# Optimization experiments

Measured on AMD Instinct MI355X. Metric: run time of the kernel, lower is better.

The kernel has to match this reference:

```python
import jax, jax.numpy as jnp
import numpy as np

MODEL_DIM = 1024
NUM_HEADS = 16
HEAD_DIM = MODEL_DIM // NUM_HEADS
B, SQ, SK = 1, 4096, 4096


def setup_inputs() -> dict:
    key = jax.random.key(0)
    ks = jax.random.split(key, 10)
    s = 0.02  # realistic init scale for weights
    inp = {
        "x_query": jax.random.normal(ks[0], (B, SQ, MODEL_DIM), jnp.float32),
        "x_context": jax.random.normal(ks[1], (B, SK, MODEL_DIM), jnp.float32),
        # causal mask [B,1,Sq,Sk]; 0 -> masked
        "mask": jnp.tril(jnp.ones((SQ, SK), jnp.int32))[None, None, :, :],
        "wq": jax.random.normal(ks[2], (MODEL_DIM, MODEL_DIM), jnp.float32) * s,
        "bq": jnp.zeros((MODEL_DIM,), jnp.float32),
        "wk": jax.random.normal(ks[3], (MODEL_DIM, MODEL_DIM), jnp.float32) * s,
        "bk": jnp.zeros((MODEL_DIM,), jnp.float32),
        "wv": jax.random.normal(ks[4], (MODEL_DIM, MODEL_DIM), jnp.float32) * s,
        "bv": jnp.zeros((MODEL_DIM,), jnp.float32),
        "wo": jax.random.normal(ks[5], (MODEL_DIM, MODEL_DIM), jnp.float32) * s,
        "bo": jnp.zeros((MODEL_DIM,), jnp.float32),
    }
    return inp


def reference(x_query, x_context, mask, wq, bq, wk, bk, wv, bv, wo, bo):
    b = x_query.shape[0]
    # torch nn.Linear: y = x @ W.T + b
    q = x_query @ wq.T + bq
    k = x_context @ wk.T + bk
    v = x_context @ wv.T + bv
    # [B, S, D] -> [B, H, S, Hd]
    def split_heads(t):
        return t.reshape(b, -1, NUM_HEADS, HEAD_DIM).transpose(0, 2, 1, 3)
    q, k, v = split_heads(q), split_heads(k), split_heads(v)
    scale = 1.0 / jnp.sqrt(jnp.asarray(HEAD_DIM, q.dtype))
    scores = jnp.einsum('bhqd,bhkd->bhqk', q, k) * scale  # [B,H,Sq,Sk]
    scores = jnp.where(mask == 0, jnp.asarray(-1e9, scores.dtype), scores)
    attn = jax.nn.softmax(scores, axis=-1)
    # dropout: eval mode (identity)
    ctx = jnp.einsum('bhqk,bhkd->bhqd', attn, v)
    ctx = ctx.transpose(0, 2, 1, 3).reshape(b, -1, MODEL_DIM)
    return ctx @ wo.T + bo
```

## Files before the change

### kernel.cpp

```cpp
#include <hip/hip_runtime.h>

typedef __bf16 bf16x8 __attribute__((ext_vector_type(8)));
typedef float f32x4 __attribute__((ext_vector_type(4)));
typedef float f32x16 __attribute__((ext_vector_type(16)));
typedef unsigned int u32x2v __attribute__((ext_vector_type(2)));

#define GLD16(gp, lp) __builtin_amdgcn_global_load_lds( \
    (const __attribute__((address_space(1))) void*)(gp), \
    (__attribute__((address_space(3))) void*)(lp), 16, 0, 0)

__device__ __forceinline__ unsigned short f2bf(float f) {
  unsigned int u = __float_as_uint(f);
  u += 0x7FFFu + ((u >> 16) & 1u);
  return (unsigned short)(u >> 16);
}

__device__ __forceinline__ unsigned int cvtpk(float lo, float hi) {
  unsigned int r;
  asm("v_cvt_pk_bf16_f32 %0, %1, %2" : "=v"(r) : "v"(lo), "v"(hi));
  return r;
}

__device__ __forceinline__ float exp2f_(float x) {
#if __has_builtin(__builtin_amdgcn_exp2f)
  return __builtin_amdgcn_exp2f(x);
#else
  float r; asm("v_exp_f32 %0, %1" : "=v"(r) : "v"(x)); return r;
#endif
}

__device__ __forceinline__ u32x2v pswap(unsigned int a, unsigned int b) {
#if __has_builtin(__builtin_amdgcn_permlane32_swap)
  u32x2v r;
  auto q = __builtin_amdgcn_permlane32_swap(a, b, false, false);
  r[0] = q[0]; r[1] = q[1];
  return r;
#else
  unsigned int pa = (unsigned int)__shfl_xor((int)a, 32);
  unsigned int pb = (unsigned int)__shfl_xor((int)b, 32);
  int hi = (threadIdx.x >> 5) & 1;
  u32x2v r;
  r[0] = hi ? pb : a;
  r[1] = hi ? b : pa;
  return r;
#endif
}

__global__ __launch_bounds__(256) void cast6(
    const float* __restrict__ xq, const float* __restrict__ xc,
    const float* __restrict__ wq, const float* __restrict__ wk,
    const float* __restrict__ wv, const float* __restrict__ wo,
    unsigned short* __restrict__ d) {
  int i = (blockIdx.x * 256 + threadIdx.x) * 4;
  const float* s; int off;
  if      (i < (4 << 20))  { s = xq; off = 0; }
  else if (i < (8 << 20))  { s = xc; off = 4 << 20; }
  else if (i < (9 << 20))  { s = wq; off = 8 << 20; }
  else if (i < (10 << 20)) { s = wk; off = 9 << 20; }
  else if (i < (11 << 20)) { s = wv; off = 10 << 20; }
  else                     { s = wo; off = 11 << 20; }
  float4 v = *(const float4*)(s + (i - off));
  ushort4 o;
  o.x = f2bf(v.x); o.y = f2bf(v.y); o.z = f2bf(v.z); o.w = f2bf(v.w);
  *(ushort4*)(d + i) = o;
}

template<int OUTF32>
__device__ __forceinline__ void gemm_body(
    const unsigned short* __restrict__ A, const unsigned short* __restrict__ B,
    const float* __restrict__ bias, void* __restrict__ C,
    int N, int K, int bm, int bn, float scale,
    unsigned short* As, unsigned short* Bs) {
  const int t = threadIdx.x;
  const int lane = t & 63, wid = t >> 6;
  const int wm = wid >> 1, wn = wid & 1;
  const int l15 = lane & 15, l4 = lane >> 4, l7 = lane & 7;

  f32x4 acc[2][4];
#pragma unroll
  for (int i = 0; i < 2; ++i)
#pragma unroll
    for (int j = 0; j < 4; ++j) acc[i][j] = (f32x4){0.f, 0.f, 0.f, 0.f};

  const char* Ab = (const char*)A;
  const char* Bb = (const char*)B;
  const int ldb = K * 2;

  for (int kt = 0; kt < K; kt += 64) {
#pragma unroll
    for (int c = 0; c < 2; ++c) {
      int id = c * 512 + t;
      int row = id >> 3;
      int ch = (id & 7) ^ (row & 7);
      const char* ga = Ab + (size_t)(bm * 128 + row) * ldb + kt * 2 + ch * 16;
      GLD16(ga, (char*)As + id * 16);
      const char* gb = Bb + (size_t)(bn * 128 + row) * ldb + kt * 2 + ch * 16;
      GLD16(gb, (char*)Bs + id * 16);
    }
    __syncthreads();
#pragma unroll
    for (int kk = 0; kk < 2; ++kk) {
      bf16x8 af[2], bfr[4];
#pragma unroll
      for (int mi = 0; mi < 2; ++mi) {
        int row = wm * 32 + mi * 16 + l15;
        int ch = (l4 + 4 * kk) ^ l7;
        af[mi] = *(const bf16x8*)((const char*)As + row * 128 + ch * 16);
      }
#pragma unroll
      for (int ni = 0; ni < 4; ++ni) {
        int row = wn * 64 + ni * 16 + l15;
        int ch = (l4 + 4 * kk) ^ l7;
        bfr[ni] = *(const bf16x8*)((const char*)Bs + row * 128 + ch * 16);
      }
#pragma unroll
      for (int mi = 0; mi < 2; ++mi)
#pragma unroll
        for (int ni = 0; ni < 4; ++ni)
          acc[mi][ni] = __builtin_amdgcn_mfma_f32_16x16x32_bf16(
              af[mi], bfr[ni], acc[mi][ni], 0, 0, 0);
    }
    __syncthreads();
  }

#pragma unroll
  for (int ni = 0; ni < 4; ++ni) {
    int col = bn * 128 + wn * 64 + ni * 16 + l15;
    float bv = bias[col];
#pragma unroll
    for (int mi = 0; mi < 2; ++mi) {
#pragma unroll
      for (int r = 0; r < 4; ++r) {
        int row = bm * 128 + wm * 32 + mi * 16 + l4 * 4 + r;
        float v = (acc[mi][ni][r] + bv) * scale;
        if (OUTF32) ((float*)C)[(size_t)row * N + col] = v;
        else ((unsigned short*)C)[(size_t)row * N + col] = f2bf(v);
      }
    }
  }
}

__global__ __launch_bounds__(512) void gemm_qkv(
    const unsigned short* __restrict__ xq, const unsigned short* __restrict__ xc,
    const unsigned short* __restrict__ wq, const unsigned short* __restrict__ wk,
    const unsigned short* __restrict__ wv,
    const float* __restrict__ bq, const float* __restrict__ bk,
    const float* __restrict__ bv,
    unsigned short* __restrict__ Qo, unsigned short* __restrict__ Ko,
    unsigned short* __restrict__ Vo) {
  __shared__ __align__(16) unsigned short As[128 * 64];
  __shared__ __align__(16) unsigned short Bs[128 * 64];
  const unsigned short* A; const unsigned short* B; const float* bias;
  unsigned short* C; float scale;
  if (blockIdx.z == 0)      { A = xq; B = wq; bias = bq; C = Qo; scale = 0.18033688011112042f; }
  else if (blockIdx.z == 1) { A = xc; B = wk; bias = bk; C = Ko; scale = 1.0f; }
  else                      { A = xc; B = wv; bias = bv; C = Vo; scale = 1.0f; }
  int flat = blockIdx.x + 8 * blockIdx.y;
  int tid = (flat & 7) * 32 + (flat >> 3);
  int bm = tid >> 3, bn = tid & 7;
  gemm_body<0>(A, B, bias, (void*)C, 1024, 1024, bm, bn, scale, As, Bs);
}

__global__ __launch_bounds__(512) void gemm_out(
    const unsigned short* __restrict__ A, const unsigned short* __restrict__ B,
    const float* __restrict__ bias, float* __restrict__ C) {
  __shared__ __align__(16) unsigned short As[64 * 64];
  __shared__ __align__(16) unsigned short Bs[128 * 64];
  int flat = blockIdx.x + 8 * blockIdx.y;
  int tid = (flat & 7) * 64 + (flat >> 3);
  const int bm = tid >> 3, bn = tid & 7;
  const int t = threadIdx.x;
  const int lane = t & 63, wid = t >> 6;
  const int wm = wid >> 2, wn = wid & 3;
  const int l15 = lane & 15, l4 = lane >> 4, l7 = lane & 7;

  f32x4 acc[2][2];
#pragma unroll
  for (int i = 0; i < 2; ++i)
#pragma unroll
    for (int j = 0; j < 2; ++j) acc[i][j] = (f32x4){0.f, 0.f, 0.f, 0.f};

  const char* Ab = (const char*)A;
  const char* Bb = (const char*)B;
  const int ldb = 2048;

  for (int kt = 0; kt < 1024; kt += 64) {
    {
      int id = t;
      int row = id >> 3;
      int ch = (id & 7) ^ (row & 7);
      const char* ga = Ab + (size_t)(bm * 64 + row) * ldb + kt * 2 + ch * 16;
      GLD16(ga, (char*)As + id * 16);
    }
#pragma unroll
    for (int c = 0; c < 2; ++c) {
      int id = c * 512 + t;
      int row = id >> 3;
      int ch = (id & 7) ^ (row & 7);
      const char* gb = Bb + (size_t)(bn * 128 + row) * ldb + kt * 2 + ch * 16;
      GLD16(gb, (char*)Bs + id * 16);
    }
    __syncthreads();
#pragma unroll
    for (int kk = 0; kk < 2; ++kk) {
      bf16x8 af[2], bfr[2];
#pragma unroll
      for (int mi = 0; mi < 2; ++mi) {
        int row = wm * 32 + mi * 16 + l15;
        int ch = (l4 + 4 * kk) ^ l7;
        af[mi] = *(const bf16x8*)((const char*)As + row * 128 + ch * 16);
      }
#pragma unroll
      for (int ni = 0; ni < 2; ++ni) {
        int row = wn * 32 + ni * 16 + l15;
        int ch = (l4 + 4 * kk) ^ l7;
        bfr[ni] = *(const bf16x8*)((const char*)Bs + row * 128 + ch * 16);
      }
#pragma unroll
      for (int mi = 0; mi < 2; ++mi)
#pragma unroll
        for (int ni = 0; ni < 2; ++ni)
          acc[mi][ni] = __builtin_amdgcn_mfma_f32_16x16x32_bf16(
              af[mi], bfr[ni], acc[mi][ni], 0, 0, 0);
    }
    __syncthreads();
  }

#pragma unroll
  for (int ni = 0; ni < 2; ++ni) {
    int col = bn * 128 + wn * 32 + ni * 16 + l15;
    float bv = bias[col];
#pragma unroll
    for (int mi = 0; mi < 2; ++mi) {
#pragma unroll
      for (int r = 0; r < 4; ++r) {
        int row = bm * 64 + wm * 32 + mi * 16 + l4 * 4 + r;
        C[(size_t)row * 1024 + col] = acc[mi][ni][r] + bv;
      }
    }
  }
}

__global__ __launch_bounds__(256)
void flash_attn(
    const unsigned short* __restrict__ Q, const unsigned short* __restrict__ K,
    const unsigned short* __restrict__ V, unsigned short* __restrict__ O,
    unsigned short* __restrict__ partO, float* __restrict__ lBase) {
  __shared__ __align__(16) char smem[32768];

  const int b = blockIdx.x;
  const int h = b & 15;
  const int ep = b >> 4;
  int qb, role, P;
  if (ep < 30)      { qb = 31 - ep / 3; role = ep % 3; P = 3; }
  else if (ep < 52) { int k = ep - 30; qb = 21 - (k >> 1); role = k & 1; P = 2; }
  else              { qb = 10 - (ep - 52); role = 0; P = 1; }

  const int T = 2 * qb + 2;
  const int t0 = (role * T) / P;
  const int n  = ((role + 1) * T) / P - t0;

  const int t = threadIdx.x;
  const int lane = t & 63, w = t >> 6;
  const int l31 = lane & 31, hi = lane >> 5;
  const int q0w = qb * 128 + w * 32;
  const int qwmax = q0w + 31;

  bf16x8 qf[4];
#pragma unroll
  for (int ks = 0; ks < 4; ++ks)
    qf[ks] = *(const bf16x8*)(Q + (size_t)(q0w + l31) * 1024 + h * 64 + ks * 16 + hi * 8);

  f32x16 po0, po1;
#pragma unroll
  for (int r = 0; r < 16; ++r) { po0[r] = 0.f; po1[r] = 0.f; }
  float lacc[8];
#pragma unroll
  for (int i = 0; i < 8; ++i) lacc[i] = 0.f;

  const int vd4 = (t & 15) * 4;
  const int vkvr = (t >> 4) * 4;
  uint2 va[4];

  auto stageK = [&](int tile, int buf) {
#pragma unroll
    for (int i = 0; i < 2; ++i) {
      int id = i * 256 + t;
      int row = id >> 3;
      int ch = (id & 7) ^ (row & 7);
      GLD16((const char*)K + (size_t)(tile * 64 + row) * 2048 + h * 128 + ch * 16,
            smem + buf * 8192 + id * 16);
    }
  };
  auto loadV = [&](int tile) {
#pragma unroll
    for (int i = 0; i < 4; ++i)
      va[i] = *(const uint2*)(V + (size_t)(tile * 64 + vkvr + i) * 1024 + h * 64 + vd4);
  };
  auto writeV = [&](int buf) {
    char* Vt = smem + 16384 + buf * 8192;
#pragma unroll
    for (int j = 0; j < 4; ++j) {
      unsigned sel = (j & 1) ? 0x07060302u : 0x05040100u;
      unsigned s01 = (j < 2) ? __builtin_amdgcn_perm(va[1].x, va[0].x, sel)
                             : __builtin_amdgcn_perm(va[1].y, va[0].y, sel);
      unsigned s23 = (j < 2) ? __builtin_amdgcn_perm(va[3].x, va[2].x, sel)
                             : __builtin_amdgcn_perm(va[3].y, va[2].y, sel);
      int row = vd4 + j;
      int sw = (vkvr * 2) ^ (((row >> 2) & 7) << 4);
      *(uint2*)(Vt + row * 128 + sw) = make_uint2(s01, s23);
    }
  };

  stageK(t0, 0);
  loadV(t0);
  writeV(0);
  __syncthreads();

  for (int it = 0; it < n; ++it) {
    const int c = it & 1;
    const bool pf = (it + 1) < n;
    if (pf) { stageK(t0 + it + 1, c ^ 1); loadV(t0 + it + 1); }

    const int kv0 = (t0 + it) * 64;
    if (kv0 <= qwmax) {
      const char* Ks = smem + c * 8192;
      const char* Vt = smem + 16384 + c * 8192;
      f32x16 s0, s1;
#pragma unroll
      for (int r = 0; r < 16; ++r) { s0[r] = 0.f; s1[r] = 0.f; }
      __builtin_amdgcn_s_setprio(1);
#pragma unroll
      for (int ks = 0; ks < 4; ++ks) {
        int c0 = ((ks * 2 + hi) ^ (l31 & 7)) << 4;
        bf16x8 k0 = *(const bf16x8*)(Ks + l31 * 128 + c0);
        bf16x8 k1 = *(const bf16x8*)(Ks + (32 + l31) * 128 + c0);
        s0 = __builtin_amdgcn_mfma_f32_32x32x16_bf16(k0, qf[ks], s0, 0, 0, 0);
        s1 = __builtin_amdgcn_mfma_f32_32x32x16_bf16(k1, qf[ks], s1, 0, 0, 0);
      }
      __builtin_amdgcn_s_setprio(0);
      if (kv0 + 63 > q0w) {
        int q = q0w + l31;
#pragma unroll
        for (int r = 0; r < 16; ++r) {
          int kvi = kv0 + (r & 3) + 8 * (r >> 2) + 4 * hi;
          if (kvi > q) s0[r] = -1e30f;
          if (kvi + 32 > q) s1[r] = -1e30f;
        }
      }
#pragma unroll
      for (int r = 0; r < 16; ++r) s0[r] = exp2f_(s0[r]);
#pragma unroll
      for (int r = 0; r < 16; ++r) s1[r] = exp2f_(s1[r]);
#pragma unroll
      for (int i = 0; i < 8; ++i)
        lacc[i] += (s0[2 * i] + s0[2 * i + 1]) + (s1[2 * i] + s1[2 * i + 1]);

#pragma unroll
      for (int kp = 0; kp < 4; ++kp) {
        const f32x16& sv = (kp < 2) ? s0 : s1;
        const int bb = (kp & 1) * 8;
        unsigned c0v = cvtpk(sv[bb + 0], sv[bb + 1]);
        unsigned c1v = cvtpk(sv[bb + 2], sv[bb + 3]);
        unsigned c2v = cvtpk(sv[bb + 4], sv[bb + 5]);
        unsigned c3v = cvtpk(sv[bb + 6], sv[bb + 7]);
        u32x2v w02 = pswap(c0v, c2v);
        u32x2v w13 = pswap(c1v, c3v);
        union { unsigned u[4]; bf16x8 v; } pfr;
        pfr.u[0] = w02[0]; pfr.u[1] = w13[0]; pfr.u[2] = w02[1]; pfr.u[3] = w13[1];
        int cb = kp * 2 + hi;
        __builtin_amdgcn_s_setprio(1);
        {
          int row = l31;
          bf16x8 vf = *(const bf16x8*)(Vt + row * 128 + ((cb ^ ((row >> 2) & 7)) << 4));
          po0 = __builtin_amdgcn_mfma_f32_32x32x16_bf16(vf, pfr.v, po0, 0, 0, 0);
        }
        {
          int row = 32 + l31;
          bf16x8 vf = *(const bf16x8*)(Vt + row * 128 + ((cb ^ ((row >> 2) & 7)) << 4));
          po1 = __builtin_amdgcn_mfma_f32_32x32x16_bf16(vf, pfr.v, po1, 0, 0, 0);
        }
        __builtin_amdgcn_s_setprio(0);
      }
    }
    if (pf) writeV(c ^ 1);
    __syncthreads();
  }

  float l4v[4];
#pragma unroll
  for (int i = 0; i < 4; ++i) l4v[i] = lacc[i] + lacc[4 + i];
  float ps = (l4v[0] + l4v[1]) + (l4v[2] + l4v[3]);
  u32x2v sw2 = pswap(__float_as_uint(ps), __float_as_uint(ps));
  const float l_i = __uint_as_float(sw2[0]) + __uint_as_float(sw2[1]);
  const float rinv = 1.0f / l_i;

  if (P > 1) {
    const int slot = h * 52 + ep;
    unsigned u[16];
#pragma unroll
    for (int i = 0; i < 8; ++i) u[i] = cvtpk(po0[2 * i] * rinv, po0[2 * i + 1] * rinv);
#pragma unroll
    for (int i = 0; i < 8; ++i) u[8 + i] = cvtpk(po1[2 * i] * rinv, po1[2 * i + 1] * rinv);
    char* bO = (char*)partO + (size_t)slot * 16384 + t * 64;
    *(uint4*)(bO +  0) = make_uint4(u[0], u[1], u[2], u[3]);
    *(uint4*)(bO + 16) = make_uint4(u[4], u[5], u[6], u[7]);
    *(uint4*)(bO + 32) = make_uint4(u[8], u[9], u[10], u[11]);
    *(uint4*)(bO + 48) = make_uint4(u[12], u[13], u[14], u[15]);
    if (!hi) {
      lBase[(size_t)slot * 128 + w * 32 + l31] = l_i;
    }
    return;
  }

  {
    int qlocal = w * 32 + l31;
#pragma unroll
    for (int g = 0; g < 4; ++g) {
#pragma unroll
      for (int db = 0; db < 2; ++db) {
        const f32x16& p = db ? po1 : po0;
        unsigned w0 = cvtpk(p[g * 4 + 0] * rinv, p[g * 4 + 1] * rinv);
        unsigned w1 = cvtpk(p[g * 4 + 2] * rinv, p[g * 4 + 3] * rinv);
        int d0 = db * 32 + 8 * g + 4 * hi;
        int byte = qlocal * 128 + ((d0 * 2) ^ ((qlocal & 7) << 4));
        *(uint2*)(smem + byte) = make_uint2(w0, w1);
      }
    }
  }
  __syncthreads();
#pragma unroll
  for (int it = 0; it < 4; ++it) {
    int r = it * 32 + (t >> 3);
    int c = t & 7;
    uint4 val = *(const uint4*)(smem + r * 128 + ((c ^ (r & 7)) << 4));
    *(uint4*)((char*)O + (size_t)(qb * 128 + r) * 2048 + h * 128 + c * 16) = val;
  }
}

__global__ __launch_bounds__(256) void flash_merge(
    const unsigned short* __restrict__ partO, const float* __restrict__ lBase,
    unsigned short* __restrict__ O) {
  const int p = blockIdx.x;
  const int h = p & 15;
  const int j = p >> 4;
  int qb, P, e0;
  if (j < 10) { qb = 31 - j; P = 3; e0 = j * 3; }
  else        { qb = 21 - (j - 10); P = 2; e0 = 30 + (j - 10) * 2; }
  const int t = threadIdx.x;
  const int s = t >> 6, hi = (t >> 5) & 1, l31 = t & 31;

  float acc[32];
#pragma unroll
  for (int i = 0; i < 32; ++i) acc[i] = 0.f;
  float den = 0.f;
#pragma unroll
  for (int r = 0; r < 3; ++r) {
    if (r < P) {
      float wgt = lBase[(size_t)(h * 52 + e0 + r) * 128 + s * 32 + l31];
      den += wgt;
      const uint4* bO = (const uint4*)((const char*)partO +
                         (size_t)(h * 52 + e0 + r) * 16384 + t * 64);
      uint4 a = bO[0], b2 = bO[1], c2 = bO[2], d2 = bO[3];
      unsigned uu[16] = {a.x, a.y, a.z, a.w, b2.x, b2.y, b2.z, b2.w,
                         c2.x, c2.y, c2.z, c2.w, d2.x, d2.y, d2.z, d2.w};
#pragma unroll
      for (int i = 0; i < 16; ++i) {
        acc[2 * i]     += wgt * __uint_as_float(uu[i] << 16);
        acc[2 * i + 1] += wgt * __uint_as_float(uu[i] & 0xFFFF0000u);
      }
    }
  }
  float rinv = 1.0f / den;
  const int q = qb * 128 + s * 32 + l31;
  unsigned short* orow = O + (size_t)q * 1024 + h * 64;
#pragma unroll
  for (int r = 0; r < 16; ++r) {
    int d = (r & 3) + 8 * (r >> 2) + 4 * hi;
    orow[d]      = f2bf(acc[r] * rinv);
    orow[d + 32] = f2bf(acc[16 + r] * rinv);
  }
}

extern "C" void kernel_launch(void* const* d_in, const int* in_sizes, int n_in,
                              void* d_out, int out_size, void* d_ws, size_t ws_size,
                              hipStream_t stream) {
  const float* xq = (const float*)d_in[0];
  const float* xc = (const float*)d_in[1];
  const float* wq = (const float*)d_in[3];
  const float* bq = (const float*)d_in[4];
  const float* wk = (const float*)d_in[5];
  const float* bk = (const float*)d_in[6];
  const float* wv = (const float*)d_in[7];
  const float* bv = (const float*)d_in[8];
  const float* wo = (const float*)d_in[9];
  const float* bo = (const float*)d_in[10];

  unsigned short* wsb = (unsigned short*)d_ws;
  unsigned short* xqb = wsb;
  unsigned short* xcb = wsb + (4 << 20);
  unsigned short* wqb = wsb + (8 << 20);
  unsigned short* wkb = wsb + (9 << 20);
  unsigned short* wvb = wsb + (10 << 20);
  unsigned short* wob = wsb + (11 << 20);
  unsigned short* Qb  = wsb + (12 << 20);
  unsigned short* Kb  = wsb + (16 << 20);
  unsigned short* Vb  = wsb + (20 << 20);
  unsigned short* Cb  = wsb + (24 << 20);

  unsigned short* partO = (unsigned short*)d_ws;
  float* lBase = (float*)((char*)d_ws + (14u << 20));

  cast6<<<12288, 256, 0, stream>>>(xq, xc, wq, wk, wv, wo, wsb);

  dim3 gq(1024 / 128, 4096 / 128, 3);
  gemm_qkv<<<gq, 512, 0, stream>>>(xqb, xcb, wqb, wkb, wvb, bq, bk, bv, Qb, Kb, Vb);

  flash_attn<<<1008, 256, 0, stream>>>(Qb, Kb, Vb, Cb, partO, lBase);

  flash_merge<<<336, 256, 0, stream>>>(partO, lBase, Cb);

  dim3 go(1024 / 128, 4096 / 64);
  gemm_out<<<go, 512, 0, stream>>>(Cb, wob, bo, (float*)d_out);
}
```

Measured before the change: 140.1 us.

## Fuse activation fp32-to-bf16 cast into QKV GEMM A-tile loads

Stops pre-casting x_query and x_context to bf16 in a separate pass. The QKV GEMM now loads fp32 A tiles straight into LDS with a new swizzle and converts them to bf16 with v_cvt_pk_bf16_f32 when building fragments. Only the weights are still cast ahead of time. This removes a 32 MB read plus 16 MB write pass. In exchange, A-tile global and LDS traffic inside the GEMM doubles, LDS use grows to 48 KB per block, and the conversion adds ALU work in the inner loop that K and V blocks repeat on the same rows.

Result: slower. 148.7 us (+6.1%).

```diff
diff --git a/kernel.cpp b/kernel.cpp
--- a/kernel.cpp
+++ b/kernel.cpp
@@ -46,111 +46,33 @@
 #endif
 }
 
-__global__ __launch_bounds__(256) void cast6(
-    const float* __restrict__ xq, const float* __restrict__ xc,
+__global__ __launch_bounds__(256) void cast_w(
     const float* __restrict__ wq, const float* __restrict__ wk,
     const float* __restrict__ wv, const float* __restrict__ wo,
     unsigned short* __restrict__ d) {
   int i = (blockIdx.x * 256 + threadIdx.x) * 4;
   const float* s; int off;
-  if      (i < (4 << 20))  { s = xq; off = 0; }
-  else if (i < (8 << 20))  { s = xc; off = 4 << 20; }
-  else if (i < (9 << 20))  { s = wq; off = 8 << 20; }
-  else if (i < (10 << 20)) { s = wk; off = 9 << 20; }
-  else if (i < (11 << 20)) { s = wv; off = 10 << 20; }
-  else                     { s = wo; off = 11 << 20; }
+  if      (i < (1 << 20)) { s = wq; off = 0; }
+  else if (i < (2 << 20)) { s = wk; off = 1 << 20; }
+  else if (i < (3 << 20)) { s = wv; off = 2 << 20; }
+  else                    { s = wo; off = 3 << 20; }
   float4 v = *(const float4*)(s + (i - off));
   ushort4 o;
   o.x = f2bf(v.x); o.y = f2bf(v.y); o.z = f2bf(v.z); o.w = f2bf(v.w);
   *(ushort4*)(d + i) = o;
 }
 
-template<int OUTF32>
-__device__ __forceinline__ void gemm_body(
-    const unsigned short* __restrict__ A, const unsigned short* __restrict__ B,
-    const float* __restrict__ bias, void* __restrict__ C,
-    int N, int K, int bm, int bn, float scale,
-    unsigned short* As, unsigned short* Bs) {
-  const int t = threadIdx.x;
-  const int lane = t & 63, wid = t >> 6;
-  const int wm = wid >> 1, wn = wid & 1;
-  const int l15 = lane & 15, l4 = lane >> 4, l7 = lane & 7;
-
-  f32x4 acc[2][4];
-#pragma unroll
-  for (int i = 0; i < 2; ++i)
-#pragma unroll
-    for (int j = 0; j < 4; ++j) acc[i][j] = (f32x4){0.f, 0.f, 0.f, 0.f};
-
-  const char* Ab = (const char*)A;
-  const char* Bb = (const char*)B;
-  const int ldb = K * 2;
-
-  for (int kt = 0; kt < K; kt += 64) {
-#pragma unroll
-    for (int c = 0; c < 2; ++c) {
-      int id = c * 512 + t;
-      int row = id >> 3;
-      int ch = (id & 7) ^ (row & 7);
-      const char* ga = Ab + (size_t)(bm * 128 + row) * ldb + kt * 2 + ch * 16;
-      GLD16(ga, (char*)As + id * 16);
-      const char* gb = Bb + (size_t)(bn * 128 + row) * ldb + kt * 2 + ch * 16;
-      GLD16(gb, (char*)Bs + id * 16);
-    }
-    __syncthreads();
-#pragma unroll
-    for (int kk = 0; kk < 2; ++kk) {
-      bf16x8 af[2], bfr[4];
-#pragma unroll
-      for (int mi = 0; mi < 2; ++mi) {
-        int row = wm * 32 + mi * 16 + l15;
-        int ch = (l4 + 4 * kk) ^ l7;
-        af[mi] = *(const bf16x8*)((const char*)As + row * 128 + ch * 16);
-      }
-#pragma unroll
-      for (int ni = 0; ni < 4; ++ni) {
-        int row = wn * 64 + ni * 16 + l15;
-        int ch = (l4 + 4 * kk) ^ l7;
-        bfr[ni] = *(const bf16x8*)((const char*)Bs + row * 128 + ch * 16);
-      }
-#pragma unroll
-      for (int mi = 0; mi < 2; ++mi)
-#pragma unroll
-        for (int ni = 0; ni < 4; ++ni)
-          acc[mi][ni] = __builtin_amdgcn_mfma_f32_16x16x32_bf16(
-              af[mi], bfr[ni], acc[mi][ni], 0, 0, 0);
-    }
-    __syncthreads();
-  }
-
-#pragma unroll
-  for (int ni = 0; ni < 4; ++ni) {
-    int col = bn * 128 + wn * 64 + ni * 16 + l15;
-    float bv = bias[col];
-#pragma unroll
-    for (int mi = 0; mi < 2; ++mi) {
-#pragma unroll
-      for (int r = 0; r < 4; ++r) {
-        int row = bm * 128 + wm * 32 + mi * 16 + l4 * 4 + r;
-        float v = (acc[mi][ni][r] + bv) * scale;
-        if (OUTF32) ((float*)C)[(size_t)row * N + col] = v;
-        else ((unsigned short*)C)[(size_t)row * N + col] = f2bf(v);
-      }
-    }
-  }
-}
-
 __global__ __launch_bounds__(512) void gemm_qkv(
-    const unsigned short* __restrict__ xq, const unsigned short* __restrict__ xc,
+    const float* __restrict__ xq, const float* __restrict__ xc,
     const unsigned short* __restrict__ wq, const unsigned short* __restrict__ wk,
     const unsigned short* __restrict__ wv,
     const float* __restrict__ bq, const float* __restrict__ bk,
     const float* __restrict__ bv,
     unsigned short* __restrict__ Qo, unsigned short* __restrict__ Ko,
     unsigned short* __restrict__ Vo) {
-  __shared__ __align__(16) unsigned short As[128 * 64];
+  __shared__ __align__(16) float As[128 * 64];
   __shared__ __align__(16) unsigned short Bs[128 * 64];
-  const unsigned short* A; const unsigned short* B; const float* bias;
+  const float* A; const unsigned short* B; const float* bias;
   unsigned short* C; float scale;
   if (blockIdx.z == 0)      { A = xq; B = wq; bias = bq; C = Qo; scale = 0.18033688011112042f; }
   else if (blockIdx.z == 1) { A = xc; B = wk; bias = bk; C = Ko; scale = 1.0f; }
@@ -158,7 +80,86 @@
   int flat = blockIdx.x + 8 * blockIdx.y;
   int tid = (flat & 7) * 32 + (flat >> 3);
   int bm = tid >> 3, bn = tid & 7;
-  gemm_body<0>(A, B, bias, (void*)C, 1024, 1024, bm, bn, scale, As, Bs);
+
+  const int t = threadIdx.x;
+  const int lane = t & 63, wid = t >> 6;
+  const int wm = wid >> 1, wn = wid & 1;
+  const int l15 = lane & 15, l4 = lane >> 4, l7 = lane & 7;
+
+  f32x4 acc[2][4];
+#pragma unroll
+  for (int i = 0; i < 2; ++i)
+#pragma unroll
+    for (int j = 0; j < 4; ++j) acc[i][j] = (f32x4){0.f, 0.f, 0.f, 0.f};
+
+  const char* Bb = (const char*)B;
+
+  for (int kt = 0; kt < 1024; kt += 64) {
+#pragma unroll
+    for (int c = 0; c < 2; ++c) {
+      int id = c * 512 + t;
+      int row = id >> 3;
+      int ch = (id & 7) ^ (row & 7);
+      GLD16(Bb + (size_t)(bn * 128 + row) * 2048 + kt * 2 + ch * 16,
+            (char*)Bs + id * 16);
+    }
+#pragma unroll
+    for (int c = 0; c < 4; ++c) {
+      int id = c * 512 + t;
+      int row = id >> 4;
+      int cc = id & 15;
+      int sc = (((cc >> 1) ^ (row & 7)) << 1) | (cc & 1);
+      GLD16(A + (size_t)(bm * 128 + row) * 1024 + kt + sc * 4,
+            (char*)As + id * 16);
+    }
+    __syncthreads();
+#pragma unroll
+    for (int kk = 0; kk < 2; ++kk) {
+      bf16x8 af[2], bfr[4];
+#pragma unroll
+      for (int mi = 0; mi < 2; ++mi) {
+        int row = wm * 32 + mi * 16 + l15;
+        int p = (l4 + 4 * kk) ^ (row & 7);
+        const char* base = (const char*)As + row * 256 + p * 32;
+        f32x4 v0 = *(const f32x4*)(base);
+        f32x4 v1 = *(const f32x4*)(base + 16);
+        union { uint4 u; bf16x8 v; } cv;
+        cv.u.x = cvtpk(v0[0], v0[1]);
+        cv.u.y = cvtpk(v0[2], v0[3]);
+        cv.u.z = cvtpk(v1[0], v1[1]);
+        cv.u.w = cvtpk(v1[2], v1[3]);
+        af[mi] = cv.v;
+      }
+#pragma unroll
+      for (int ni = 0; ni < 4; ++ni) {
+        int row = wn * 64 + ni * 16 + l15;
+        int ch = (l4 + 4 * kk) ^ l7;
+        bfr[ni] = *(const bf16x8*)((const char*)Bs + row * 128 + ch * 16);
+      }
+#pragma unroll
+      for (int mi = 0; mi < 2; ++mi)
+#pragma unroll
+        for (int ni = 0; ni < 4; ++ni)
+          acc[mi][ni] = __builtin_amdgcn_mfma_f32_16x16x32_bf16(
+              af[mi], bfr[ni], acc[mi][ni], 0, 0, 0);
+    }
+    __syncthreads();
+  }
+
+#pragma unroll
+  for (int ni = 0; ni < 4; ++ni) {
+    int col = bn * 128 + wn * 64 + ni * 16 + l15;
+    float bv = bias[col];
+#pragma unroll
+    for (int mi = 0; mi < 2; ++mi) {
+#pragma unroll
+      for (int r = 0; r < 4; ++r) {
+        int row = bm * 128 + wm * 32 + mi * 16 + l4 * 4 + r;
+        float v = (acc[mi][ni][r] + bv) * scale;
+        C[(size_t)row * 1024 + col] = f2bf(v);
+      }
+    }
+  }
 }
 
 __global__ __launch_bounds__(512) void gemm_out(
@@ -497,8 +498,6 @@
   const float* bo = (const float*)d_in[10];
 
   unsigned short* wsb = (unsigned short*)d_ws;
-  unsigned short* xqb = wsb;
-  unsigned short* xcb = wsb + (4 << 20);
   unsigned short* wqb = wsb + (8 << 20);
   unsigned short* wkb = wsb + (9 << 20);
   unsigned short* wvb = wsb + (10 << 20);
@@ -511,10 +510,10 @@
   unsigned short* partO = (unsigned short*)d_ws;
   float* lBase = (float*)((char*)d_ws + (14u << 20));
 
-  cast6<<<12288, 256, 0, stream>>>(xq, xc, wq, wk, wv, wo, wsb);
+  cast_w<<<4096, 256, 0, stream>>>(wq, wk, wv, wo, wqb);
 
   dim3 gq(1024 / 128, 4096 / 128, 3);
-  gemm_qkv<<<gq, 512, 0, stream>>>(xqb, xcb, wqb, wkb, wvb, bq, bk, bv, Qb, Kb, Vb);
+  gemm_qkv<<<gq, 512, 0, stream>>>(xq, xc, wqb, wkb, wvb, bq, bk, bv, Qb, Kb, Vb);
 
   flash_attn<<<1008, 256, 0, stream>>>(Qb, Kb, Vb, Cb, partO, lBase);
 
```
